# Kernel optimization log

Hardware: AMD Instinct MI355X
Metric: run time of the kernel (lower is better)

## Reference

```python
import jax, jax.numpy as jnp
import numpy as np

N_NODES, N_EDGES, D_IN, D_HID, D_OUT = 100000, 3200000, 128, 64, 10


def _gcn_norm(src, dst, n):
    # symmetric normalization deg^{-1/2}[src] * deg^{-1/2}[dst]; edge weights = 1
    ones = jnp.ones(src.shape[0], jnp.float32)
    deg = jax.ops.segment_sum(ones, dst, num_segments=n)
    dinv = jnp.where(deg > 0, jax.lax.rsqrt(jnp.maximum(deg, 1.0)), 0.0)
    return dinv[src] * dinv[dst]


def _gcn_conv(x, W, b, src, dst, norm, n):
    h = x @ W                                   # [N, out]
    msg = norm[:, None] * jnp.take(h, src, axis=0)  # [E+N, out]
    return jax.ops.segment_sum(msg, dst, num_segments=n) + b


def setup_inputs() -> dict:
    key = jax.random.key(0)
    ks = jax.random.split(key, 8)
    x = jax.random.normal(ks[0], (N_NODES, D_IN), jnp.float32)
    edge_index = jax.random.randint(ks[1], (2, N_EDGES), 0, N_NODES, jnp.int32)
    def glorot(k, fan_in, fan_out):
        s = (6.0 / (fan_in + fan_out)) ** 0.5
        return jax.random.uniform(k, (fan_in, fan_out), jnp.float32, -s, s)
    return {
        "x": x,
        "edge_index": edge_index,
        "W1": glorot(ks[2], D_IN, D_HID), "b1": jnp.zeros((D_HID,), jnp.float32),
        "W2": glorot(ks[3], D_HID, D_HID), "b2": jnp.zeros((D_HID,), jnp.float32),
        "W3": glorot(ks[4], D_HID, D_OUT), "b3": jnp.zeros((D_OUT,), jnp.float32),
    }


def reference(x, edge_index, W1, b1, W2, b2, W3, b3):
    n = x.shape[0]
    loops = jnp.arange(n, dtype=edge_index.dtype)
    src = jnp.concatenate([edge_index[0], loops])  # add self-loops (PyG default)
    dst = jnp.concatenate([edge_index[1], loops])
    norm = _gcn_norm(src, dst, n)                  # identical for all 3 layers
    h = jax.nn.relu(_gcn_conv(x, W1, b1, src, dst, norm, n))
    h = jax.nn.relu(_gcn_conv(h, W2, b2, src, dst, norm, n))
    return _gcn_conv(h, W3, b3, src, dst, norm, n)
```

## Files before the change

### kernel.cpp

```cpp
#include <hip/hip_runtime.h>


constexpr int BK_SHIFT = 6;
constexpr int BK_NODES = 64;
constexpr int BK_CAP   = 2432;
constexpr int MAXNB    = 1568;

typedef __attribute__((ext_vector_type(8))) short short8_t;
typedef __attribute__((ext_vector_type(4))) float f32x4_t;

__device__ __forceinline__ unsigned short f2bf(float f) {
    unsigned u = __builtin_bit_cast(unsigned, f);
    u += 0x7FFF + ((u >> 16) & 1);
    return (unsigned short)(u >> 16);
}
__device__ __forceinline__ unsigned pack2(float lo, float hi) {
    return (unsigned)f2bf(lo) | ((unsigned)f2bf(hi) << 16);
}
__device__ __forceinline__ float bf_lo(unsigned d) {
    return __builtin_bit_cast(float, d << 16);
}
__device__ __forceinline__ float bf_hi(unsigned d) {
    return __builtin_bit_cast(float, d & 0xFFFF0000u);
}
__device__ __forceinline__ float bf1(unsigned short u) {
    return __builtin_bit_cast(float, (unsigned)u << 16);
}

__global__ __launch_bounds__(512) void k_partition(const int* __restrict__ src,
                            const int* __restrict__ dst,
                            int E, int nb, int* __restrict__ cursor,
                            unsigned* __restrict__ inter) {
    __shared__ int lcount[MAXNB];
    __shared__ int gbase[MAXNB];
    int t = threadIdx.x;
    int base = blockIdx.x * 16384;
    for (int i = t; i < MAXNB; i += 512) lcount[i] = 0;
    __syncthreads();
    unsigned rec[32];
    unsigned meta[32];
    int rem = E - base;
    if (rem >= 16384) {
        const int4* src4 = reinterpret_cast<const int4*>(src + base);
        const int4* dst4 = reinterpret_cast<const int4*>(dst + base);
#pragma unroll
        for (int j = 0; j < 8; j++) {
            int4 s4 = src4[j * 512 + t];
            int4 d4 = dst4[j * 512 + t];
            int ss[4] = {s4.x, s4.y, s4.z, s4.w};
            int dd[4] = {d4.x, d4.y, d4.z, d4.w};
#pragma unroll
            for (int k = 0; k < 4; k++) {
                int b = dd[k] >> BK_SHIFT;
                int r = atomicAdd(&lcount[b], 1);
                rec[j * 4 + k] = (unsigned)ss[k] | ((unsigned)(dd[k] & (BK_NODES - 1)) << 20);
                meta[j * 4 + k] = (unsigned)b | ((unsigned)r << 11);
            }
        }
    } else {
#pragma unroll
        for (int j = 0; j < 32; j++) {
            int idx = base + j * 512 + t;
            if (idx < E) {
                int s = src[idx], d = dst[idx];
                int b = d >> BK_SHIFT;
                int r = atomicAdd(&lcount[b], 1);
                rec[j] = (unsigned)s | ((unsigned)(d & (BK_NODES - 1)) << 20);
                meta[j] = (unsigned)b | ((unsigned)r << 11);
            } else meta[j] = 0xFFFFFFFFu;
        }
    }
    __syncthreads();
    for (int i = t; i < nb; i += 512) {
        int c = lcount[i];
        gbase[i] = c ? atomicAdd(&cursor[i], c) : 0;
    }
    __syncthreads();
    if (rem >= 16384) {
#pragma unroll
        for (int j = 0; j < 32; j++) {
            int b = meta[j] & 2047;
            int pos = gbase[b] + (int)(meta[j] >> 11);
            if (pos < BK_CAP) inter[(size_t)b * BK_CAP + pos] = rec[j];
        }
    } else {
#pragma unroll
        for (int j = 0; j < 32; j++) {
            if (meta[j] != 0xFFFFFFFFu) {
                int b = meta[j] & 2047;
                int pos = gbase[b] + (int)(meta[j] >> 11);
                if (pos < BK_CAP) inter[(size_t)b * BK_CAP + pos] = rec[j];
            }
        }
    }
}

__global__ __launch_bounds__(512) void k_sort(const unsigned* __restrict__ inter,
                        const int* __restrict__ cursor,
                        unsigned* __restrict__ srt_g, int* __restrict__ offs_g,
                        float* __restrict__ dinv, int N) {
    __shared__ unsigned raw[BK_CAP];
    __shared__ unsigned srt[BK_CAP];
    __shared__ int hist[BK_NODES];
    __shared__ int offs[BK_NODES + 1];
    __shared__ int cur[BK_NODES];
    int t = threadIdx.x, b = blockIdx.x;
    if (t < BK_NODES) hist[t] = 0;
    __syncthreads();
    int cnt = min(cursor[b], BK_CAP);
    const unsigned* ip = inter + (size_t)b * BK_CAP;
    int c4 = cnt & ~3;
    for (int i = t * 4; i < c4; i += 2048) {
        uint4 r4 = *reinterpret_cast<const uint4*>(ip + i);
        *reinterpret_cast<uint4*>(&raw[i]) = r4;
        atomicAdd(&hist[r4.x >> 20], 1);
        atomicAdd(&hist[r4.y >> 20], 1);
        atomicAdd(&hist[r4.z >> 20], 1);
        atomicAdd(&hist[r4.w >> 20], 1);
    }
    for (int i = c4 + t; i < cnt; i += 512) {
        unsigned r = ip[i];
        raw[i] = r;
        atomicAdd(&hist[r >> 20], 1);
    }
    __syncthreads();
    if (t < BK_NODES) {
        int v = hist[t];
        int inc = v;
#pragma unroll
        for (int d = 1; d < 64; d <<= 1) {
            int o = __shfl_up(inc, d);
            if (t >= d) inc += o;
        }
        offs[t + 1] = inc;
        if (t == 0) offs[0] = 0;
        cur[t] = inc - v;
        int d = b * BK_NODES + t;
        if (d < N) dinv[d] = rsqrtf((float)(v + 1));
    }
    __syncthreads();
    for (int i = t; i < cnt; i += 512) {
        unsigned r = raw[i];
        int pos = atomicAdd(&cur[r >> 20], 1);
        srt[pos] = r & 0xFFFFFu;
    }
    __syncthreads();
    unsigned* sg = srt_g + (size_t)b * BK_CAP;
    for (int i = t * 4; i < c4; i += 2048)
        *reinterpret_cast<uint4*>(sg + i) = *reinterpret_cast<const uint4*>(&srt[i]);
    for (int i = c4 + t; i < cnt; i += 512) sg[i] = srt[i];
    if (t < BK_NODES + 1) offs_g[b * (BK_NODES + 1) + t] = offs[t];
}

template <int K, bool IN_F32>
__global__ __launch_bounds__(256) void k_gemmMF(const void* __restrict__ Xv,
                           const float* __restrict__ W,
                           const float* __restrict__ dinv,
                           unsigned short* __restrict__ Y, int n) {
    constexpr int KP = K + 8;
    __shared__ unsigned short Al[64 * KP];
    __shared__ unsigned short Bl[64 * KP];
    int t = threadIdx.x;
    int nb = blockIdx.x * 64;
    if (IN_F32) {
        const float* X = (const float*)Xv;
        for (int i = t * 4; i < 64 * K; i += 1024) {
            int r = i / K, c = i % K;
            int node = nb + r;
            float4 v = {0.f, 0.f, 0.f, 0.f};
            if (node < n) v = *reinterpret_cast<const float4*>(X + (size_t)node * K + c);
            uint2 pk = {pack2(v.x, v.y), pack2(v.z, v.w)};
            *reinterpret_cast<uint2*>(&Al[r * KP + c]) = pk;
        }
    } else {
        const unsigned short* X = (const unsigned short*)Xv;
        for (int i = t * 4; i < 64 * K; i += 1024) {
            int r = i / K, c = i % K;
            int node = nb + r;
            uint2 pk = {0u, 0u};
            if (node < n) pk = *reinterpret_cast<const uint2*>(X + (size_t)node * K + c);
            *reinterpret_cast<uint2*>(&Al[r * KP + c]) = pk;
        }
    }
    {
        int c = t & 63, kb = t >> 6;
        for (int k = kb; k < K; k += 4)
            Bl[c * KP + k] = f2bf(W[k * 64 + c]);
    }
    __syncthreads();
    int w = t >> 6, lane = t & 63;
    int ml = lane & 15, kg = lane >> 4;
    f32x4_t acc[4] = {{0,0,0,0},{0,0,0,0},{0,0,0,0},{0,0,0,0}};
    for (int ks = 0; ks < K / 32; ks++) {
        int ko = ks * 32 + kg * 8;
        short8_t a = *reinterpret_cast<const short8_t*>(&Al[(16 * w + ml) * KP + ko]);
#pragma unroll
        for (int c = 0; c < 4; c++) {
            short8_t b = *reinterpret_cast<const short8_t*>(&Bl[(16 * c + ml) * KP + ko]);
            acc[c] = __builtin_amdgcn_mfma_f32_16x16x32_bf16(a, b, acc[c], 0, 0, 0);
        }
    }
#pragma unroll
    for (int r = 0; r < 4; r++) {
        int grow = nb + 16 * w + kg * 4 + r;
        if (grow < n) {
            float dv = dinv[grow];
#pragma unroll
            for (int c = 0; c < 4; c++)
                Y[(size_t)grow * 64 + 16 * c + ml] = f2bf(dv * acc[c][r]);
        }
    }
}

__global__ void k_gemm10(const float* __restrict__ X, const float* __restrict__ W,
                         const float* __restrict__ dinv, unsigned short* __restrict__ Y, int n) {
    __shared__ float ws[64 * 10];
    __shared__ float xs[16 * 64];
    int t = threadIdx.x;
    for (int i = t; i < 640; i += 256) ws[i] = W[i];
    int nb = blockIdx.x * 16;
    for (int i = t; i < 16 * 64; i += 256) {
        int r = i >> 6, c = i & 63;
        int node = nb + r;
        xs[i] = (node < n) ? X[(size_t)node * 64 + c] : 0.f;
    }
    __syncthreads();
    int ns = t >> 4, c = t & 15;
    if (c < 10) {
        float acc = 0.f;
        for (int k = 0; k < 64; k++) acc += xs[ns * 64 + k] * ws[k * 10 + c];
        int node = nb + ns;
        if (node < n) Y[(size_t)node * 10 + c] = f2bf(dinv[node] * acc);
    }
}

template <int OBF>
__global__ __launch_bounds__(512) void k_agg64(const unsigned short* __restrict__ H,
                        const unsigned* __restrict__ srt_g, const int* __restrict__ offs_g,
                        const float* __restrict__ dinv, const float* __restrict__ bias,
                        void* __restrict__ outv, int N, int relu) {
    __shared__ unsigned srt[BK_CAP];
    __shared__ int offs[BK_NODES + 1];
    int t = threadIdx.x, b = blockIdx.x;
    if (t < BK_NODES + 1) offs[t] = offs_g[b * (BK_NODES + 1) + t];
    __syncthreads();
    int cnt = offs[BK_NODES];
    const unsigned* sg = srt_g + (size_t)b * BK_CAP;
    int c4 = cnt & ~3;
    for (int i = t * 4; i < c4; i += 2048)
        *reinterpret_cast<uint4*>(&srt[i]) = *reinterpret_cast<const uint4*>(sg + i);
    for (int i = c4 + t; i < cnt; i += 512) srt[i] = sg[i];
    __syncthreads();
    int wv = t >> 6, lane = t & 63;
    int esub = lane >> 3, cg = lane & 7;
    const unsigned short* Hc = H + (cg << 3);
    for (int nd = wv; nd < BK_NODES; nd += 8) {
        int d = b * BK_NODES + nd;
        if (d >= N) break;
        int o0 = offs[nd], o1 = offs[nd + 1];
        uint4 sv = {0, 0, 0, 0};
        float dv = 0.f;
        if (esub == 0) {
            sv = *reinterpret_cast<const uint4*>(Hc + ((size_t)d << 6));
            dv = dinv[d];
        }
        float a0 = 0.f, a1 = 0.f, a2 = 0.f, a3 = 0.f;
        float a4 = 0.f, a5 = 0.f, a6 = 0.f, a7 = 0.f;
        int e = o0 + esub;
        for (; e + 8 < o1; e += 16) {
            int s0 = srt[e], s1 = srt[e + 8];
            const uint4 v0 = *reinterpret_cast<const uint4*>(Hc + ((size_t)s0 << 6));
            const uint4 v1 = *reinterpret_cast<const uint4*>(Hc + ((size_t)s1 << 6));
            a0 += bf_lo(v0.x); a1 += bf_hi(v0.x); a2 += bf_lo(v0.y); a3 += bf_hi(v0.y);
            a4 += bf_lo(v0.z); a5 += bf_hi(v0.z); a6 += bf_lo(v0.w); a7 += bf_hi(v0.w);
            a0 += bf_lo(v1.x); a1 += bf_hi(v1.x); a2 += bf_lo(v1.y); a3 += bf_hi(v1.y);
            a4 += bf_lo(v1.z); a5 += bf_hi(v1.z); a6 += bf_lo(v1.w); a7 += bf_hi(v1.w);
        }
        if (e < o1) {
            int s0 = srt[e];
            const uint4 v0 = *reinterpret_cast<const uint4*>(Hc + ((size_t)s0 << 6));
            a0 += bf_lo(v0.x); a1 += bf_hi(v0.x); a2 += bf_lo(v0.y); a3 += bf_hi(v0.y);
            a4 += bf_lo(v0.z); a5 += bf_hi(v0.z); a6 += bf_lo(v0.w); a7 += bf_hi(v0.w);
        }
#pragma unroll
        for (int m = 8; m <= 32; m <<= 1) {
            a0 += __shfl_xor(a0, m); a1 += __shfl_xor(a1, m);
            a2 += __shfl_xor(a2, m); a3 += __shfl_xor(a3, m);
            a4 += __shfl_xor(a4, m); a5 += __shfl_xor(a5, m);
            a6 += __shfl_xor(a6, m); a7 += __shfl_xor(a7, m);
        }
        if (esub == 0) {
            float s[8] = {bf_lo(sv.x), bf_hi(sv.x), bf_lo(sv.y), bf_hi(sv.y),
                          bf_lo(sv.z), bf_hi(sv.z), bf_lo(sv.w), bf_hi(sv.w)};
            float ac[8] = {a0, a1, a2, a3, a4, a5, a6, a7};
            const float* bp = bias + cg * 8;
            float o[8];
#pragma unroll
            for (int j = 0; j < 8; j++) {
                float val = dv * (ac[j] + s[j]) + bp[j];
                if (relu) val = fmaxf(val, 0.f);
                o[j] = val;
            }
            if (OBF) {
                unsigned short* op = (unsigned short*)outv + (size_t)d * 64 + cg * 8;
                uint4 pk = {pack2(o[0], o[1]), pack2(o[2], o[3]),
                            pack2(o[4], o[5]), pack2(o[6], o[7])};
                *reinterpret_cast<uint4*>(op) = pk;
            } else {
                float* op = (float*)outv + (size_t)d * 64 + cg * 8;
                float4 r0 = {o[0], o[1], o[2], o[3]}, r1 = {o[4], o[5], o[6], o[7]};
                *reinterpret_cast<float4*>(op)     = r0;
                *reinterpret_cast<float4*>(op + 4) = r1;
            }
        }
    }
}

__global__ __launch_bounds__(512) void k_agg10s(const unsigned short* __restrict__ H,
                        const unsigned* __restrict__ srt_g, const int* __restrict__ offs_g,
                        const float* __restrict__ dinv, const float* __restrict__ b3,
                        float* __restrict__ out, int N) {
    __shared__ unsigned srt[BK_CAP];
    __shared__ int offs[BK_NODES + 1];
    int t = threadIdx.x, b = blockIdx.x;
    if (t < BK_NODES + 1) offs[t] = offs_g[b * (BK_NODES + 1) + t];
    __syncthreads();
    int cnt = offs[BK_NODES];
    const unsigned* sg = srt_g + (size_t)b * BK_CAP;
    int c4 = cnt & ~3;
    for (int i = t * 4; i < c4; i += 2048)
        *reinterpret_cast<uint4*>(&srt[i]) = *reinterpret_cast<const uint4*>(sg + i);
    for (int i = c4 + t; i < cnt; i += 512) srt[i] = sg[i];
    __syncthreads();
    int wv = t >> 6, lane = t & 63;
    int es = lane >> 4, c = lane & 15;
    for (int nd = wv; nd < BK_NODES; nd += 8) {
        int d = b * BK_NODES + nd;
        if (d >= N) break;
        int o0 = offs[nd], o1 = offs[nd + 1];
        float acc = 0.f;
        if (c < 10) {
            int e = o0 + es;
            for (; e + 4 < o1; e += 8) {
                int s0 = srt[e], s1 = srt[e + 4];
                acc += bf1(H[(size_t)s0 * 10 + c]) + bf1(H[(size_t)s1 * 10 + c]);
            }
            if (e < o1) acc += bf1(H[(size_t)srt[e] * 10 + c]);
        }
        acc += __shfl_xor(acc, 16);
        acc += __shfl_xor(acc, 32);
        if (es == 0 && c < 10) {
            float dv = dinv[d];
            out[(size_t)d * 10 + c] = dv * (acc + bf1(H[(size_t)d * 10 + c])) + b3[c];
        }
    }
}

extern "C" void kernel_launch(void* const* d_in, const int* in_sizes, int n_in,
                              void* d_out, int out_size, void* d_ws, size_t ws_size,
                              hipStream_t stream) {
    const float* x  = (const float*)d_in[0];
    const int*   ei = (const int*)d_in[1];
    const float* W1 = (const float*)d_in[2];
    const float* b1 = (const float*)d_in[3];
    const float* W2 = (const float*)d_in[4];
    const float* b2 = (const float*)d_in[5];
    const float* W3 = (const float*)d_in[6];
    const float* b3 = (const float*)d_in[7];

    int N = in_sizes[0] / 128;
    int E = in_sizes[1] / 2;
    const int* esrc = ei;
    const int* edst = ei + E;
    int nb = (N + BK_NODES - 1) >> BK_SHIFT;

    char* p = (char*)d_ws;
    auto carve = [&](size_t bytes) -> void* {
        void* r = p;
        p += (bytes + 255) & ~(size_t)255;
        return r;
    };
    int*      cursor = (int*)carve((size_t)MAXNB * 4);
    unsigned* inter  = (unsigned*)carve((size_t)nb * BK_CAP * 4);
    unsigned* srt_g  = (unsigned*)carve((size_t)nb * BK_CAP * 4);
    int*      offs_g = (int*)carve((size_t)nb * (BK_NODES + 1) * 4);
    float*    dinv   = (float*)carve((size_t)N * 4);
    unsigned short* Hs = (unsigned short*)carve((size_t)N * 64 * 2);
    unsigned short* Gb = (unsigned short*)carve((size_t)N * 64 * 2);
    float*    Gf     = (float*)carve((size_t)N * 64 * 4);
    unsigned short* Hs10 = (unsigned short*)carve((size_t)N * 10 * 2);
    (void)ws_size; (void)n_in; (void)out_size;

    hipMemsetAsync(cursor, 0, (size_t)nb * 4, stream);
    k_partition<<<(E + 16383) / 16384, 512, 0, stream>>>(esrc, edst, E, nb, cursor, inter);
    k_sort<<<nb, 512, 0, stream>>>(inter, cursor, srt_g, offs_g, dinv, N);

    k_gemmMF<128, true><<<(N + 63) / 64, 256, 0, stream>>>(x, W1, dinv, Hs, N);
    k_agg64<1><<<nb, 512, 0, stream>>>(Hs, srt_g, offs_g, dinv, b1, Gb, N, 1);
    k_gemmMF<64, false><<<(N + 63) / 64, 256, 0, stream>>>(Gb, W2, dinv, Hs, N);
    k_agg64<0><<<nb, 512, 0, stream>>>(Hs, srt_g, offs_g, dinv, b2, Gf, N, 1);
    k_gemm10<<<(N + 15) / 16, 256, 0, stream>>>(Gf, W3, dinv, Hs10, N);
    k_agg10s<<<nb, 512, 0, stream>>>(Hs10, srt_g, offs_g, dinv, b3, (float*)d_out, N);
}
```

Baseline: 239.7 us.

## Double node bucket size and pad final-layer features to 16 for vector gathers

Bucket granularity grows from 64 to 128 nodes per block with larger capacity, and the in-block prefix scan moves from a single-wavefront shuffle to a shared-memory Hillis-Steele scan. The 10-wide final-layer feature rows are padded to 16 bf16 values so each lane gathers four channels with one 8-byte load instead of scalar 2-byte loads. Bigger buckets mean fewer blocks and more shared memory per block, which can lower occupancy for the sort and aggregate kernels. The padding adds extra bytes per row in return for aligned vector gathers.

```diff
diff --git a/kernel.cpp b/kernel.cpp
--- a/kernel.cpp
+++ b/kernel.cpp
@@ -1,10 +1,10 @@
 #include <hip/hip_runtime.h>
 
 
-constexpr int BK_SHIFT = 6;
-constexpr int BK_NODES = 64;
-constexpr int BK_CAP   = 2432;
-constexpr int MAXNB    = 1568;
+constexpr int BK_SHIFT = 7;
+constexpr int BK_NODES = 128;
+constexpr int BK_CAP   = 4688;
+constexpr int MAXNB    = 784;
 
 typedef __attribute__((ext_vector_type(8))) short short8_t;
 typedef __attribute__((ext_vector_type(4))) float f32x4_t;
@@ -102,6 +102,7 @@
     __shared__ unsigned raw[BK_CAP];
     __shared__ unsigned srt[BK_CAP];
     __shared__ int hist[BK_NODES];
+    __shared__ int tmp[BK_NODES];
     __shared__ int offs[BK_NODES + 1];
     __shared__ int cur[BK_NODES];
     int t = threadIdx.x, b = blockIdx.x;
@@ -124,19 +125,21 @@
         atomicAdd(&hist[r >> 20], 1);
     }
     __syncthreads();
+    if (t < BK_NODES) tmp[t] = hist[t];
+    __syncthreads();
+    for (int st = 1; st < BK_NODES; st <<= 1) {
+        int v = 0;
+        if (t < BK_NODES && t >= st) v = tmp[t - st];
+        __syncthreads();
+        if (t < BK_NODES) tmp[t] += v;
+        __syncthreads();
+    }
     if (t < BK_NODES) {
-        int v = hist[t];
-        int inc = v;
-#pragma unroll
-        for (int d = 1; d < 64; d <<= 1) {
-            int o = __shfl_up(inc, d);
-            if (t >= d) inc += o;
-        }
-        offs[t + 1] = inc;
+        offs[t + 1] = tmp[t];
         if (t == 0) offs[0] = 0;
-        cur[t] = inc - v;
+        cur[t] = tmp[t] - hist[t];
         int d = b * BK_NODES + t;
-        if (d < N) dinv[d] = rsqrtf((float)(v + 1));
+        if (d < N) dinv[d] = rsqrtf((float)(hist[t] + 1));
     }
     __syncthreads();
     for (int i = t; i < cnt; i += 512) {
@@ -226,11 +229,15 @@
     }
     __syncthreads();
     int ns = t >> 4, c = t & 15;
-    if (c < 10) {
-        float acc = 0.f;
-        for (int k = 0; k < 64; k++) acc += xs[ns * 64 + k] * ws[k * 10 + c];
-        int node = nb + ns;
-        if (node < n) Y[(size_t)node * 10 + c] = f2bf(dinv[node] * acc);
+    int node = nb + ns;
+    if (node < n) {
+        unsigned short o = 0;
+        if (c < 10) {
+            float acc = 0.f;
+            for (int k = 0; k < 64; k++) acc += xs[ns * 64 + k] * ws[k * 10 + c];
+            o = f2bf(dinv[node] * acc);
+        }
+        Y[(size_t)node * 16 + c] = o;
     }
 }
 
@@ -333,25 +340,47 @@
     for (int i = c4 + t; i < cnt; i += 512) srt[i] = sg[i];
     __syncthreads();
     int wv = t >> 6, lane = t & 63;
-    int es = lane >> 4, c = lane & 15;
+    int es = lane >> 2, cg = lane & 3;
+    const unsigned short* Hc = H + cg * 4;
     for (int nd = wv; nd < BK_NODES; nd += 8) {
         int d = b * BK_NODES + nd;
         if (d >= N) break;
         int o0 = offs[nd], o1 = offs[nd + 1];
-        float acc = 0.f;
-        if (c < 10) {
-            int e = o0 + es;
-            for (; e + 4 < o1; e += 8) {
-                int s0 = srt[e], s1 = srt[e + 4];
-                acc += bf1(H[(size_t)s0 * 10 + c]) + bf1(H[(size_t)s1 * 10 + c]);
+        uint2 sv = {0, 0};
+        float dv = 0.f;
+        if (es == 0) {
+            sv = *reinterpret_cast<const uint2*>(Hc + (size_t)d * 16);
+            dv = dinv[d];
+        }
+        float a0 = 0.f, a1 = 0.f, a2 = 0.f, a3 = 0.f;
+        int e = o0 + es;
+        for (; e + 16 < o1; e += 32) {
+            int s0 = srt[e], s1 = srt[e + 16];
+            const uint2 v0 = *reinterpret_cast<const uint2*>(Hc + (size_t)s0 * 16);
+            const uint2 v1 = *reinterpret_cast<const uint2*>(Hc + (size_t)s1 * 16);
+            a0 += bf_lo(v0.x) + bf_lo(v1.x); a1 += bf_hi(v0.x) + bf_hi(v1.x);
+            a2 += bf_lo(v0.y) + bf_lo(v1.y); a3 += bf_hi(v0.y) + bf_hi(v1.y);
+        }
+        if (e < o1) {
+            int s0 = srt[e];
+            const uint2 v0 = *reinterpret_cast<const uint2*>(Hc + (size_t)s0 * 16);
+            a0 += bf_lo(v0.x); a1 += bf_hi(v0.x);
+            a2 += bf_lo(v0.y); a3 += bf_hi(v0.y);
+        }
+#pragma unroll
+        for (int m = 4; m <= 32; m <<= 1) {
+            a0 += __shfl_xor(a0, m); a1 += __shfl_xor(a1, m);
+            a2 += __shfl_xor(a2, m); a3 += __shfl_xor(a3, m);
+        }
+        if (es == 0) {
+            float s[4] = {bf_lo(sv.x), bf_hi(sv.x), bf_lo(sv.y), bf_hi(sv.y)};
+            float ac[4] = {a0, a1, a2, a3};
+#pragma unroll
+            for (int j = 0; j < 4; j++) {
+                int ch = cg * 4 + j;
+                if (ch < 10)
+                    out[(size_t)d * 10 + ch] = dv * (ac[j] + s[j]) + b3[ch];
             }
-            if (e < o1) acc += bf1(H[(size_t)srt[e] * 10 + c]);
-        }
-        acc += __shfl_xor(acc, 16);
-        acc += __shfl_xor(acc, 32);
-        if (es == 0 && c < 10) {
-            float dv = dinv[d];
-            out[(size_t)d * 10 + c] = dv * (acc + bf1(H[(size_t)d * 10 + c])) + b3[c];
         }
     }
 }
@@ -388,7 +417,7 @@
     unsigned short* Hs = (unsigned short*)carve((size_t)N * 64 * 2);
     unsigned short* Gb = (unsigned short*)carve((size_t)N * 64 * 2);
     float*    Gf     = (float*)carve((size_t)N * 64 * 4);
-    unsigned short* Hs10 = (unsigned short*)carve((size_t)N * 10 * 2);
+    unsigned short* Hs10 = (unsigned short*)carve((size_t)N * 16 * 2);
     (void)ws_size; (void)n_in; (void)out_size;
 
     hipMemsetAsync(cursor, 0, (size_t)nb * 4, stream);
```

Measured after the change: 250.5 us. 4.5% more time.
